# Kernel optimization log

Hardware: AMD Instinct MI355X
Metric: run time of the kernel (lower is better)

The kernel has to match this reference:

```python
import jax, jax.numpy as jnp
import numpy as np

H = 32        # num_attention_heads
KVH = 8       # num_key_value_heads
D = 64        # attention_head_size
WIN = 256     # attention_window_size (left/right)
ROPE_BASE = 10000.0


def setup_inputs() -> dict:
    key = jax.random.key(0)
    k1, k2, k3 = jax.random.split(key, 3)
    B, S = 2, 2048
    return {
        "query_states": jax.random.normal(k1, (B, S, H * D), dtype=jnp.float32),
        "key_states": jax.random.normal(k2, (B, S, KVH * D), dtype=jnp.float32),
        "value_states": jax.random.normal(k3, (B, S, KVH * D), dtype=jnp.float32),
    }


def _rope_cos_sin(seq_len, dtype):
    inv_freq = 1.0 / (ROPE_BASE ** (jnp.arange(0, D, 2, dtype=jnp.float32) / D))  # [D/2]
    pos = jnp.arange(seq_len, dtype=jnp.float32)
    freqs = pos[:, None] * inv_freq[None, :]          # [S, D/2]
    emb = jnp.concatenate([freqs, freqs], axis=-1)    # [S, D]
    return jnp.cos(emb).astype(dtype), jnp.sin(emb).astype(dtype)


def _rotate_half(x):
    x1, x2 = x[..., : D // 2], x[..., D // 2 :]
    return jnp.concatenate([-x2, x1], axis=-1)


def reference(query_states, key_states, value_states):
    B, S, _ = query_states.shape
    n_rep = H // KVH

    q = query_states.reshape(B, S, H, D).transpose(0, 2, 1, 3)        # [B,H,S,D]
    k = key_states.reshape(B, S, KVH, D).transpose(0, 2, 1, 3)        # [B,KVH,S,D]
    v = value_states.reshape(B, S, KVH, D).transpose(0, 2, 1, 3)

    # repeat_kv: [B,KVH,S,D] -> [B,H,S,D]
    k = jnp.repeat(k, n_rep, axis=1)
    v = jnp.repeat(v, n_rep, axis=1)

    cos, sin = _rope_cos_sin(S, q.dtype)   # [S,D]
    cos = cos[None, None]                  # [1,1,S,D]
    sin = sin[None, None]
    q = q * cos + _rotate_half(q) * sin
    k = k * cos + _rotate_half(k) * sin

    scale = 1.0 / jnp.sqrt(jnp.asarray(D, dtype=q.dtype))
    scores = jnp.einsum("bhqd,bhkd->bhqk", q, k) * scale              # [B,H,S,S]

    i = jnp.arange(S)[:, None]
    j = jnp.arange(S)[None, :]
    allowed = (j >= i - WIN) & (j <= i)                               # [S,S]
    scores = jnp.where(allowed[None, None], scores, jnp.finfo(scores.dtype).min)

    probs = jax.nn.softmax(scores, axis=-1)
    out = jnp.einsum("bhqk,bhkd->bhqd", probs, v)                     # [B,H,S,D]
    return out.transpose(0, 2, 1, 3).reshape(B, S, H * D)
```

## Files before the change

### kernel.cpp

```cpp
#include <hip/hip_runtime.h>
#include <math.h>

#define NH   32
#define NKVH 8
#define HD   64
#define WIN  256
#define BB   2
#define SS   2048

typedef short short8 __attribute__((ext_vector_type(8)));
typedef float f32x4  __attribute__((ext_vector_type(4)));

__device__ __forceinline__ ushort f2bf(float x) {
    union { float f; unsigned u; } v; v.f = x;
    unsigned u = v.u + 0x7FFF + ((v.u >> 16) & 1);
    return (ushort)(u >> 16);
}

__global__ __launch_bounds__(256) void prep_kv(const float* __restrict__ K,
                                               const float* __restrict__ V,
                                               ushort* __restrict__ Kr,
                                               ushort* __restrict__ Vt) {
    __shared__ ushort tile[64][65];
    int bidx = blockIdx.x;
    int s0  = (bidx & 31) * 64;
    int kvh = (bidx >> 5) & 7;
    int b   = bidx >> 8;
    int d   = threadIdx.x & 63, g = threadIdx.x >> 6;

    float inv = __powf(10000.f, -(float)(d & 31) * (1.f / 32.f));
#pragma unroll
    for (int i = 0; i < 16; ++i) {
        int s = s0 + g * 16 + i;
        float kv = K[(size_t)(b * SS + s) * (NKVH * HD) + kvh * HD + d];
        float partner = __shfl(kv, d ^ 32, 64);
        float sn, cs;
        __sincosf((float)s * inv, &sn, &cs);
        float krot = kv * cs + ((d < 32) ? -partner : partner) * sn;
        Kr[((size_t)(b * NKVH + kvh) * SS + s) * HD + d] = f2bf(krot);
    }
#pragma unroll
    for (int i = 0; i < 16; ++i) {
        int sl = g * 16 + i;
        tile[sl][d] = f2bf(V[(size_t)(b * SS + s0 + sl) * (NKVH * HD) + kvh * HD + d]);
    }
    __syncthreads();
#pragma unroll
    for (int i = 0; i < 16; ++i) {
        int dr = g * 16 + i;
        Vt[((size_t)(b * NKVH + kvh) * HD + dr) * SS + s0 + d] = tile[d][dr];
    }
}

__global__ __launch_bounds__(256, 4) void attn_mfma(const float* __restrict__ Q,
                                                    const ushort* __restrict__ Kr,
                                                    const ushort* __restrict__ Vt,
                                                    float* __restrict__ O) {
    __shared__ ushort Pl[4][2][2][16][40];
    const int wv = threadIdx.x >> 6, lane = threadIdx.x & 63;
    const int lo16 = lane & 15, quad = lane >> 4;
    const int bidx = blockIdx.x;
    const int qblk = bidx & 63;
    const int kvh  = (bidx >> 6) & 7;
    const int b    = bidx >> 9;
    const int h    = kvh * 4 + wv;
    const int q0   = qblk * 32;

    float invf[8];
#pragma unroll
    for (int j = 0; j < 8; ++j)
        invf[j] = __powf(10000.f, -(float)(quad * 8 + j) * (1.f / 32.f));

    short8 aq[2][2];
#pragma unroll
    for (int t = 0; t < 2; ++t) {
        int qi = q0 + t * 16 + lo16;
        const float* qrow = Q + (size_t)(b * SS + qi) * (NH * HD) + h * HD;
        float lo[8], hi[8];
        *(float4*)(lo)     = *(const float4*)(qrow + quad * 8);
        *(float4*)(lo + 4) = *(const float4*)(qrow + quad * 8 + 4);
        *(float4*)(hi)     = *(const float4*)(qrow + 32 + quad * 8);
        *(float4*)(hi + 4) = *(const float4*)(qrow + 32 + quad * 8 + 4);
#pragma unroll
        for (int j = 0; j < 8; ++j) {
            float sn, cs;
            __sincosf((float)qi * invf[j], &sn, &cs);
            aq[t][0][j] = (short)f2bf((lo[j] * cs - hi[j] * sn) * 0.125f);
            aq[t][1][j] = (short)f2bf((hi[j] * cs + lo[j] * sn) * 0.125f);
        }
    }

    const ushort* kbase = Kr + (size_t)(b * NKVH + kvh) * SS * HD;
    const ushort* vbase = Vt + (size_t)(b * NKVH + kvh) * HD * SS;

    f32x4 acc[2][4];
#pragma unroll
    for (int t = 0; t < 2; ++t)
#pragma unroll
        for (int i = 0; i < 4; ++i) acc[t][i] = (f32x4){0.f, 0.f, 0.f, 0.f};
    float psum[2] = {0.f, 0.f};

    int klo = q0 - WIN; if (klo < 0) klo = 0;
    const int khi = q0 + 31;

    short8 kcur[4], knxt[4];
    {
        int key0 = klo + lo16, key1 = klo + 16 + lo16;
        kcur[0] = *(const short8*)(kbase + (size_t)key0 * HD + quad * 8);
        kcur[1] = *(const short8*)(kbase + (size_t)key0 * HD + 32 + quad * 8);
        kcur[2] = *(const short8*)(kbase + (size_t)key1 * HD + quad * 8);
        kcur[3] = *(const short8*)(kbase + (size_t)key1 * HD + 32 + quad * 8);
    }

    int buf = 0;
    for (int kb = klo; kb <= khi; kb += 32, buf ^= 1) {
        const f32x4 z = {0.f, 0.f, 0.f, 0.f};
        f32x4 s00 = __builtin_amdgcn_mfma_f32_16x16x32_bf16(kcur[0], aq[0][0], z,   0, 0, 0);
        s00       = __builtin_amdgcn_mfma_f32_16x16x32_bf16(kcur[1], aq[0][1], s00, 0, 0, 0);
        f32x4 s01 = __builtin_amdgcn_mfma_f32_16x16x32_bf16(kcur[2], aq[0][0], z,   0, 0, 0);
        s01       = __builtin_amdgcn_mfma_f32_16x16x32_bf16(kcur[3], aq[0][1], s01, 0, 0, 0);
        f32x4 s10 = __builtin_amdgcn_mfma_f32_16x16x32_bf16(kcur[0], aq[1][0], z,   0, 0, 0);
        s10       = __builtin_amdgcn_mfma_f32_16x16x32_bf16(kcur[1], aq[1][1], s10, 0, 0, 0);
        f32x4 s11 = __builtin_amdgcn_mfma_f32_16x16x32_bf16(kcur[2], aq[1][0], z,   0, 0, 0);
        s11       = __builtin_amdgcn_mfma_f32_16x16x32_bf16(kcur[3], aq[1][1], s11, 0, 0, 0);

#pragma unroll
        for (int t = 0; t < 2; ++t) {
            const f32x4 sa = t ? s10 : s00;
            const f32x4 sb = t ? s11 : s01;
            const int qtmin = q0 + t * 16;
            const int myq   = qtmin + lo16;
            float p[8];
            if ((kb + 31 > qtmin) || (kb < qtmin + 15 - WIN)) {
#pragma unroll
                for (int r = 0; r < 4; ++r) {
                    int key0 = kb + quad * 4 + r;
                    int key1 = key0 + 16;
                    p[r]     = (key0 <= myq && key0 >= myq - WIN) ? __expf(sa[r]) : 0.f;
                    p[4 + r] = (key1 <= myq && key1 >= myq - WIN) ? __expf(sb[r]) : 0.f;
                }
            } else {
#pragma unroll
                for (int r = 0; r < 4; ++r) { p[r] = __expf(sa[r]); p[4 + r] = __expf(sb[r]); }
            }
            psum[t] += ((p[0] + p[1]) + (p[2] + p[3])) + ((p[4] + p[5]) + (p[6] + p[7]));
            ushort4 u0 = make_ushort4(f2bf(p[0]), f2bf(p[1]), f2bf(p[2]), f2bf(p[3]));
            ushort4 u1 = make_ushort4(f2bf(p[4]), f2bf(p[5]), f2bf(p[6]), f2bf(p[7]));
            *(ushort4*)&Pl[wv][buf][t][lo16][quad * 4]      = u0;
            *(ushort4*)&Pl[wv][buf][t][lo16][16 + quad * 4] = u1;
        }

        {
            int key0 = kb + 32 + lo16; if (key0 > SS - 1) key0 = SS - 1;
            int key1 = key0 + 16;      if (key1 > SS - 1) key1 = SS - 1;
            knxt[0] = *(const short8*)(kbase + (size_t)key0 * HD + quad * 8);
            knxt[1] = *(const short8*)(kbase + (size_t)key0 * HD + 32 + quad * 8);
            knxt[2] = *(const short8*)(kbase + (size_t)key1 * HD + quad * 8);
            knxt[3] = *(const short8*)(kbase + (size_t)key1 * HD + 32 + quad * 8);
        }
        short8 vf[4];
        {
            int sb2 = kb + quad * 8; if (sb2 > SS - 8) sb2 = SS - 8;
#pragma unroll
            for (int i = 0; i < 4; ++i)
                vf[i] = *(const short8*)(vbase + (size_t)(i * 16 + lo16) * SS + sb2);
        }

        __asm__ volatile("s_waitcnt lgkmcnt(0)" ::: "memory");
        short8 ap0 = *(const short8*)&Pl[wv][buf][0][lo16][quad * 8];
        short8 ap1 = *(const short8*)&Pl[wv][buf][1][lo16][quad * 8];

#pragma unroll
        for (int i = 0; i < 4; ++i)
            acc[0][i] = __builtin_amdgcn_mfma_f32_16x16x32_bf16(ap0, vf[i], acc[0][i], 0, 0, 0);
#pragma unroll
        for (int i = 0; i < 4; ++i)
            acc[1][i] = __builtin_amdgcn_mfma_f32_16x16x32_bf16(ap1, vf[i], acc[1][i], 0, 0, 0);

#pragma unroll
        for (int i = 0; i < 4; ++i) kcur[i] = knxt[i];
    }

#pragma unroll
    for (int t = 0; t < 2; ++t) {
        float ps = psum[t];
        ps += __shfl_xor(ps, 16, 64);
        ps += __shfl_xor(ps, 32, 64);
#pragma unroll
        for (int r = 0; r < 4; ++r) {
            float invr = 1.f / __shfl(ps, quad * 4 + r, 16);
            int qr = q0 + t * 16 + quad * 4 + r;
            size_t orow = ((size_t)(b * SS + qr) * NH + h) * HD;
            O[orow + 0 * 16 + lo16] = acc[t][0][r] * invr;
            O[orow + 1 * 16 + lo16] = acc[t][1][r] * invr;
            O[orow + 2 * 16 + lo16] = acc[t][2][r] * invr;
            O[orow + 3 * 16 + lo16] = acc[t][3][r] * invr;
        }
    }
}

__device__ __forceinline__ float wave_sum(float x) {
#pragma unroll
    for (int off = 32; off > 0; off >>= 1) x += __shfl_xor(x, off, 64);
    return x;
}

__global__ __launch_bounds__(256) void attn_scalar(const float* __restrict__ Q,
                                                   const float* __restrict__ K,
                                                   const float* __restrict__ V,
                                                   float* __restrict__ O) {
    int wave = blockIdx.x * 4 + (threadIdx.x >> 6);
    int lane = threadIdx.x & 63;
    int q  = wave % SS;
    int bh = wave / SS;
    int h  = bh % NH;
    int b  = bh / NH;
    int kvh = h >> 2;

    float inv = __powf(10000.f, -(float)(lane & 31) * (1.f / 32.f));
    float sn, cs;
    __sincosf((float)q * inv, &sn, &cs);

    float qv = Q[(size_t)(b * SS + q) * (NH * HD) + h * HD + lane];
    float qpart = __shfl(qv, lane ^ 32, 64);
    float qrot = (qv * cs + ((lane < 32) ? -qpart : qpart) * sn) * 0.125f;

    const float* vbase = V + (size_t)b * SS * (NKVH * HD) + kvh * HD;
    float m = -1e30f, l = 0.f, acc = 0.f;
    int k0 = q - WIN; if (k0 < 0) k0 = 0;
    for (int k = k0; k <= q; ++k) {
        float kraw = K[(size_t)(b * SS + k) * (NKVH * HD) + kvh * HD + lane];
        float kpart = __shfl(kraw, lane ^ 32, 64);
        float ksn, kcs;
        __sincosf((float)k * inv, &ksn, &kcs);
        float kv = kraw * kcs + ((lane < 32) ? -kpart : kpart) * ksn;
        float vv = vbase[(size_t)k * (NKVH * HD) + lane];
        float score = wave_sum(qrot * kv);
        float mnew  = fmaxf(m, score);
        float alpha = __expf(m - mnew);
        float p     = __expf(score - mnew);
        l   = l * alpha + p;
        acc = acc * alpha + p * vv;
        m   = mnew;
    }
    O[(((size_t)(b * SS + q) * NH) + h) * HD + lane] = acc / l;
}

extern "C" void kernel_launch(void* const* d_in, const int* in_sizes, int n_in,
                              void* d_out, int out_size, void* d_ws, size_t ws_size,
                              hipStream_t stream) {
    const float* Q = (const float*)d_in[0];
    const float* K = (const float*)d_in[1];
    const float* V = (const float*)d_in[2];
    float* O = (float*)d_out;

    size_t kv_elems = (size_t)BB * NKVH * SS * HD;
    size_t need = 2 * kv_elems * sizeof(ushort);

    if (ws_size >= need) {
        ushort* Kr = (ushort*)d_ws;
        ushort* Vt = Kr + kv_elems;
        prep_kv<<<BB * NKVH * (SS / 64), 256, 0, stream>>>(K, V, Kr, Vt);
        attn_mfma<<<BB * NKVH * (SS / 32), 256, 0, stream>>>(Q, Kr, Vt, O);
    } else {
        attn_scalar<<<(BB * NH * SS) / 4, 256, 0, stream>>>(Q, K, V, O);
    }
}
```

Before: 133.7 us.

## Register-resident P via bpermute, prefetch V, swizzle blocks, widen prep kernel

The attention kernel no longer stages probabilities through LDS. It packs them with v_cvt_pk_bf16_f32 and redistributes them across lanes with ds_bpermute, and it double-buffers V fragments alongside K so next-tile loads are issued before the softmax math. It also adds s_setprio around the MFMA groups, remaps block indices so consecutive blocks span different heads and batches, and lowers the launch-bounds occupancy hint from 4 to 3. The prep kernel moves to 1024 threads with fewer rows per thread and interleaved K/V loads. Register pressure rises, and the block remap changes L2 locality.

```diff
diff --git a/kernel.cpp b/kernel.cpp
--- a/kernel.cpp
+++ b/kernel.cpp
@@ -17,49 +17,57 @@
     return (ushort)(u >> 16);
 }
 
-__global__ __launch_bounds__(256) void prep_kv(const float* __restrict__ K,
-                                               const float* __restrict__ V,
-                                               ushort* __restrict__ Kr,
-                                               ushort* __restrict__ Vt) {
+__device__ __forceinline__ int cvtpk_bf16(float lo, float hi) {
+    int r;
+    asm("v_cvt_pk_bf16_f32 %0, %1, %2" : "=v"(r) : "v"(lo), "v"(hi));
+    return r;
+}
+
+__global__ __launch_bounds__(1024) void prep_kv(const float* __restrict__ K,
+                                                const float* __restrict__ V,
+                                                ushort* __restrict__ Kr,
+                                                ushort* __restrict__ Vt) {
     __shared__ ushort tile[64][65];
-    int bidx = blockIdx.x;
-    int s0  = (bidx & 31) * 64;
-    int kvh = (bidx >> 5) & 7;
-    int b   = bidx >> 8;
-    int d   = threadIdx.x & 63, g = threadIdx.x >> 6;
-
-    float inv = __powf(10000.f, -(float)(d & 31) * (1.f / 32.f));
-#pragma unroll
-    for (int i = 0; i < 16; ++i) {
-        int s = s0 + g * 16 + i;
-        float kv = K[(size_t)(b * SS + s) * (NKVH * HD) + kvh * HD + d];
-        float partner = __shfl(kv, d ^ 32, 64);
+    const int bidx = blockIdx.x;
+    const int s0  = (bidx & 31) * 64;
+    const int kvh = (bidx >> 5) & 7;
+    const int b   = bidx >> 8;
+    const int d = threadIdx.x & 63, g = threadIdx.x >> 6;
+
+    const float inv = __powf(10000.f, -(float)(d & 31) * (1.f / 32.f));
+
+    float kv[4], vv[4];
+#pragma unroll
+    for (int i = 0; i < 4; ++i) {
+        int s = s0 + g * 4 + i;
+        kv[i] = K[(size_t)(b * SS + s) * (NKVH * HD) + kvh * HD + d];
+        vv[i] = V[(size_t)(b * SS + s) * (NKVH * HD) + kvh * HD + d];
+    }
+#pragma unroll
+    for (int i = 0; i < 4; ++i) {
+        int s = s0 + g * 4 + i;
+        float partner = __shfl(kv[i], d ^ 32, 64);
         float sn, cs;
         __sincosf((float)s * inv, &sn, &cs);
-        float krot = kv * cs + ((d < 32) ? -partner : partner) * sn;
+        float krot = kv[i] * cs + ((d < 32) ? -partner : partner) * sn;
         Kr[((size_t)(b * NKVH + kvh) * SS + s) * HD + d] = f2bf(krot);
-    }
-#pragma unroll
-    for (int i = 0; i < 16; ++i) {
-        int sl = g * 16 + i;
-        tile[sl][d] = f2bf(V[(size_t)(b * SS + s0 + sl) * (NKVH * HD) + kvh * HD + d]);
+        tile[g * 4 + i][d] = f2bf(vv[i]);
     }
     __syncthreads();
 #pragma unroll
-    for (int i = 0; i < 16; ++i) {
-        int dr = g * 16 + i;
+    for (int i = 0; i < 4; ++i) {
+        int dr = g * 4 + i;
         Vt[((size_t)(b * NKVH + kvh) * HD + dr) * SS + s0 + d] = tile[d][dr];
     }
 }
 
-__global__ __launch_bounds__(256, 4) void attn_mfma(const float* __restrict__ Q,
+__global__ __launch_bounds__(256, 3) void attn_mfma(const float* __restrict__ Q,
                                                     const ushort* __restrict__ Kr,
                                                     const ushort* __restrict__ Vt,
                                                     float* __restrict__ O) {
-    __shared__ ushort Pl[4][2][2][16][40];
     const int wv = threadIdx.x >> 6, lane = threadIdx.x & 63;
     const int lo16 = lane & 15, quad = lane >> 4;
-    const int bidx = blockIdx.x;
+    const int bidx = (blockIdx.x & 7) * 128 + (blockIdx.x >> 3);
     const int qblk = bidx & 63;
     const int kvh  = (bidx >> 6) & 7;
     const int b    = bidx >> 9;
@@ -100,21 +108,29 @@
         for (int i = 0; i < 4; ++i) acc[t][i] = (f32x4){0.f, 0.f, 0.f, 0.f};
     float psum[2] = {0.f, 0.f};
 
+    const int idxAB = (lo16 + ((quad & 1) << 5)) << 2;
+    const int idxCD = idxAB + 64;
+    const bool hiq  = quad >= 2;
+
     int klo = q0 - WIN; if (klo < 0) klo = 0;
     const int khi = q0 + 31;
 
-    short8 kcur[4], knxt[4];
+    short8 kcur[4], vcur[4];
     {
         int key0 = klo + lo16, key1 = klo + 16 + lo16;
         kcur[0] = *(const short8*)(kbase + (size_t)key0 * HD + quad * 8);
         kcur[1] = *(const short8*)(kbase + (size_t)key0 * HD + 32 + quad * 8);
         kcur[2] = *(const short8*)(kbase + (size_t)key1 * HD + quad * 8);
         kcur[3] = *(const short8*)(kbase + (size_t)key1 * HD + 32 + quad * 8);
-    }
-
-    int buf = 0;
-    for (int kb = klo; kb <= khi; kb += 32, buf ^= 1) {
+        int sb2 = klo + quad * 8;
+#pragma unroll
+        for (int i = 0; i < 4; ++i)
+            vcur[i] = *(const short8*)(vbase + (size_t)(i * 16 + lo16) * SS + sb2);
+    }
+
+    for (int kb = klo; kb <= khi; kb += 32) {
         const f32x4 z = {0.f, 0.f, 0.f, 0.f};
+        __builtin_amdgcn_s_setprio(1);
         f32x4 s00 = __builtin_amdgcn_mfma_f32_16x16x32_bf16(kcur[0], aq[0][0], z,   0, 0, 0);
         s00       = __builtin_amdgcn_mfma_f32_16x16x32_bf16(kcur[1], aq[0][1], s00, 0, 0, 0);
         f32x4 s01 = __builtin_amdgcn_mfma_f32_16x16x32_bf16(kcur[2], aq[0][0], z,   0, 0, 0);
@@ -123,7 +139,23 @@
         s10       = __builtin_amdgcn_mfma_f32_16x16x32_bf16(kcur[1], aq[1][1], s10, 0, 0, 0);
         f32x4 s11 = __builtin_amdgcn_mfma_f32_16x16x32_bf16(kcur[2], aq[1][0], z,   0, 0, 0);
         s11       = __builtin_amdgcn_mfma_f32_16x16x32_bf16(kcur[3], aq[1][1], s11, 0, 0, 0);
-
+        __builtin_amdgcn_s_setprio(0);
+
+        short8 knxt[4], vnxt[4];
+        {
+            int key0 = kb + 32 + lo16; if (key0 > SS - 1) key0 = SS - 1;
+            int key1 = key0 + 16;      if (key1 > SS - 1) key1 = SS - 1;
+            knxt[0] = *(const short8*)(kbase + (size_t)key0 * HD + quad * 8);
+            knxt[1] = *(const short8*)(kbase + (size_t)key0 * HD + 32 + quad * 8);
+            knxt[2] = *(const short8*)(kbase + (size_t)key1 * HD + quad * 8);
+            knxt[3] = *(const short8*)(kbase + (size_t)key1 * HD + 32 + quad * 8);
+            int sb2 = kb + 32 + quad * 8; if (sb2 > SS - 8) sb2 = SS - 8;
+#pragma unroll
+            for (int i = 0; i < 4; ++i)
+                vnxt[i] = *(const short8*)(vbase + (size_t)(i * 16 + lo16) * SS + sb2);
+        }
+
+        short8 ap[2];
 #pragma unroll
         for (int t = 0; t < 2; ++t) {
             const f32x4 sa = t ? s10 : s00;
@@ -144,41 +176,38 @@
                 for (int r = 0; r < 4; ++r) { p[r] = __expf(sa[r]); p[4 + r] = __expf(sb[r]); }
             }
             psum[t] += ((p[0] + p[1]) + (p[2] + p[3])) + ((p[4] + p[5]) + (p[6] + p[7]));
-            ushort4 u0 = make_ushort4(f2bf(p[0]), f2bf(p[1]), f2bf(p[2]), f2bf(p[3]));
-            ushort4 u1 = make_ushort4(f2bf(p[4]), f2bf(p[5]), f2bf(p[6]), f2bf(p[7]));
-            *(ushort4*)&Pl[wv][buf][t][lo16][quad * 4]      = u0;
-            *(ushort4*)&Pl[wv][buf][t][lo16][16 + quad * 4] = u1;
-        }
-
-        {
-            int key0 = kb + 32 + lo16; if (key0 > SS - 1) key0 = SS - 1;
-            int key1 = key0 + 16;      if (key1 > SS - 1) key1 = SS - 1;
-            knxt[0] = *(const short8*)(kbase + (size_t)key0 * HD + quad * 8);
-            knxt[1] = *(const short8*)(kbase + (size_t)key0 * HD + 32 + quad * 8);
-            knxt[2] = *(const short8*)(kbase + (size_t)key1 * HD + quad * 8);
-            knxt[3] = *(const short8*)(kbase + (size_t)key1 * HD + 32 + quad * 8);
-        }
-        short8 vf[4];
-        {
-            int sb2 = kb + quad * 8; if (sb2 > SS - 8) sb2 = SS - 8;
-#pragma unroll
-            for (int i = 0; i < 4; ++i)
-                vf[i] = *(const short8*)(vbase + (size_t)(i * 16 + lo16) * SS + sb2);
-        }
-
-        __asm__ volatile("s_waitcnt lgkmcnt(0)" ::: "memory");
-        short8 ap0 = *(const short8*)&Pl[wv][buf][0][lo16][quad * 8];
-        short8 ap1 = *(const short8*)&Pl[wv][buf][1][lo16][quad * 8];
-
+
+            int w0 = cvtpk_bf16(p[0], p[1]);
+            int w1 = cvtpk_bf16(p[2], p[3]);
+            int w2 = cvtpk_bf16(p[4], p[5]);
+            int w3 = cvtpk_bf16(p[6], p[7]);
+            int a0 = __builtin_amdgcn_ds_bpermute(idxAB, w0);
+            int a2 = __builtin_amdgcn_ds_bpermute(idxAB, w2);
+            int b1 = __builtin_amdgcn_ds_bpermute(idxAB, w1);
+            int b3 = __builtin_amdgcn_ds_bpermute(idxAB, w3);
+            int c0 = __builtin_amdgcn_ds_bpermute(idxCD, w0);
+            int c2 = __builtin_amdgcn_ds_bpermute(idxCD, w2);
+            int d1 = __builtin_amdgcn_ds_bpermute(idxCD, w1);
+            int d3 = __builtin_amdgcn_ds_bpermute(idxCD, w3);
+            union { int i[4]; short8 s; } u;
+            u.i[0] = hiq ? a2 : a0;
+            u.i[1] = hiq ? b3 : b1;
+            u.i[2] = hiq ? c2 : c0;
+            u.i[3] = hiq ? d3 : d1;
+            ap[t] = u.s;
+        }
+
+        __builtin_amdgcn_s_setprio(1);
 #pragma unroll
         for (int i = 0; i < 4; ++i)
-            acc[0][i] = __builtin_amdgcn_mfma_f32_16x16x32_bf16(ap0, vf[i], acc[0][i], 0, 0, 0);
+            acc[0][i] = __builtin_amdgcn_mfma_f32_16x16x32_bf16(ap[0], vcur[i], acc[0][i], 0, 0, 0);
 #pragma unroll
         for (int i = 0; i < 4; ++i)
-            acc[1][i] = __builtin_amdgcn_mfma_f32_16x16x32_bf16(ap1, vf[i], acc[1][i], 0, 0, 0);
-
-#pragma unroll
-        for (int i = 0; i < 4; ++i) kcur[i] = knxt[i];
+            acc[1][i] = __builtin_amdgcn_mfma_f32_16x16x32_bf16(ap[1], vcur[i], acc[1][i], 0, 0, 0);
+        __builtin_amdgcn_s_setprio(0);
+
+#pragma unroll
+        for (int i = 0; i < 4; ++i) { kcur[i] = knxt[i]; vcur[i] = vnxt[i]; }
     }
 
 #pragma unroll
@@ -260,7 +289,7 @@
     if (ws_size >= need) {
         ushort* Kr = (ushort*)d_ws;
         ushort* Vt = Kr + kv_elems;
-        prep_kv<<<BB * NKVH * (SS / 64), 256, 0, stream>>>(K, V, Kr, Vt);
+        prep_kv<<<BB * NKVH * (SS / 64), 1024, 0, stream>>>(K, V, Kr, Vt);
         attn_mfma<<<BB * NKVH * (SS / 32), 256, 0, stream>>>(Q, Kr, Vt, O);
     } else {
         attn_scalar<<<(BB * NH * SS) / 4, 256, 0, stream>>>(Q, K, V, O);
```

After: 149.5 us. 1.12x slower.
